# Optimization experiments

Measured on AMD Instinct MI355X. Metric: run time of the kernel, lower is better.

## Reference

```python
import jax, jax.numpy as jnp
import numpy as np

B, SQ, SK = 2, 2048, 2048   # batch, n_query, n_memory
D, H, DFF = 1024, 16, 1024  # model dim, heads, ffn dim (must equal D per source constraints)
DH = D // H                 # head dim = 64
NEG = 1e9


def _split_heads(x):
    # (B, S, D) -> (B, H, S, DH)
    b, s, _ = x.shape
    return x.reshape(b, s, H, DH).transpose(0, 2, 1, 3)


def setup_inputs() -> dict:
    key = jax.random.key(0)
    ks = jax.random.split(key, 10)
    s = 0.02
    return {
        "q": jax.random.normal(ks[0], (B, SQ, D), jnp.float32),
        "k": jax.random.normal(ks[1], (B, SK, D), jnp.float32),
        "v": jax.random.normal(ks[2], (B, SK, D), jnp.float32),
        "Win_w": jax.random.normal(ks[3], (DFF, D), jnp.float32) * s,
        "Win_b": jnp.zeros((DFF,), jnp.float32),
        "Wff_w": jax.random.normal(ks[4], (D, DFF), jnp.float32) * s,
        "Wff_b": jnp.zeros((D,), jnp.float32),
        "Wout_w": jax.random.normal(ks[5], (D, D), jnp.float32) * s,
        "Wout_b": jnp.zeros((D,), jnp.float32),
        "attn_mask": jax.random.randint(ks[6], (B, SK), 0, 2, jnp.int32),
    }


def reference(q, k, v, Win_w, Win_b, Wff_w, Wff_b, Wout_w, Wout_b, attn_mask):
    # projections (in_linear; k,v additionally pass through out_linear as in source)
    qh = q @ Win_w.T + Win_b
    kh = (k @ Win_w.T + Win_b) @ Wout_w.T + Wout_b
    vh = (v @ Win_w.T + Win_b) @ Wout_w.T + Wout_b
    qh = qh * (D ** -0.5)

    qh, kh, vh = _split_heads(qh), _split_heads(kh), _split_heads(vh)

    # additive mask bias: 0 where mask==1, -1e9 where mask==0, broadcast over heads/queries
    bias = (attn_mask.astype(jnp.float32) - 1.0) * NEG  # (B, SK)
    scores = jnp.einsum("bhqd,bhkd->bhqk", qh, kh) + bias[:, None, None, :]
    probs = jax.nn.softmax(scores, axis=-1)
    out = jnp.einsum("bhqk,bhkd->bhqd", probs, vh)

    # merge heads: (B, H, SQ, DH) -> (B, SQ, D)
    out = out.transpose(0, 2, 1, 3).reshape(B, SQ, D)

    out = out @ Wff_w.T + Wff_b
    out = out @ Wout_w.T + Wout_b
    return out
```

## Files before the change

kernel.cpp:

```cpp
#include <hip/hip_runtime.h>
#include <cstdint>
#include <cstddef>

using u16 = unsigned short;
using u32 = unsigned int;

typedef __attribute__((ext_vector_type(8))) short short8;
typedef __attribute__((ext_vector_type(4))) float f32x4;

#define MFMA16(a, b, c) __builtin_amdgcn_mfma_f32_16x16x32_bf16((a), (b), (c), 0, 0, 0)

#define QSCALE 0.0450842200f

__device__ __forceinline__ u16 f2bf(float f) {
  u32 u = __float_as_uint(f);
  return (u16)((u + 0x7FFFu + ((u >> 16) & 1u)) >> 16);
}

__device__ __forceinline__ u32 pack_bf16(float a, float b) {
  u32 r;
  asm("v_cvt_pk_bf16_f32 %0, %1, %2" : "=v"(r) : "v"(a), "v"(b));
  return r;
}

__device__ __forceinline__ void gload_lds16(const u16* g, u16* l) {
  __builtin_amdgcn_global_load_lds((const __attribute__((address_space(1))) void*)g,
                                   (__attribute__((address_space(3))) void*)l, 16, 0, 0);
}

__global__ __launch_bounds__(256) void prep_all(
    const float* __restrict__ q, const float* __restrict__ k, const float* __restrict__ v,
    const float* __restrict__ Wout_w, const float* __restrict__ Win_w,
    const float* __restrict__ Wff_w, const float* __restrict__ Win_b,
    const float* __restrict__ Wout_b, u16* __restrict__ X,
    u16* __restrict__ Woutb, u16* __restrict__ Winb,
    u16* __restrict__ WinT, u16* __restrict__ WffT,
    float* __restrict__ bias2, float* __restrict__ bias1f) {
  __shared__ float tile[64][68];
  const int t = threadIdx.x;
  const int bid = blockIdx.x;
  if (bid < 12288) {
    int i4 = bid * 256 + t;
    const float* src = (i4 < 1048576) ? q : (i4 < 2097152) ? k : v;
    int loc = i4 & 1048575;
    float4 w = reinterpret_cast<const float4*>(src)[loc];
    u32 lo = (u32)f2bf(w.x) | ((u32)f2bf(w.y) << 16);
    u32 hi = (u32)f2bf(w.z) | ((u32)f2bf(w.w) << 16);
    reinterpret_cast<uint2*>(X)[i4] = make_uint2(lo, hi);
  } else if (bid < 14336) {
    const int wb = bid - 12288;
    const float* src = wb < 1024 ? Wout_w : Win_w;
    u16* dst = wb < 1024 ? Woutb : Winb;
    const float sc = wb < 1024 ? 1.0f : QSCALE;
    int i = (wb & 1023) * 256 + t;
    float4 vv = reinterpret_cast<const float4*>(src)[i];
    u32 lo = (u32)f2bf(vv.x * sc) | ((u32)f2bf(vv.y * sc) << 16);
    u32 hi = (u32)f2bf(vv.z * sc) | ((u32)f2bf(vv.w * sc) << 16);
    reinterpret_cast<uint2*>(dst)[i] = make_uint2(lo, hi);
  } else if (bid < 14848) {
    const int tb = bid - 14336;
    const float* in = tb < 256 ? Win_w : Wff_w;
    u16* out = tb < 256 ? WinT : WffT;
    const int tix = tb & 255;
    const int bx = (tix >> 4) * 64, by = (tix & 15) * 64;
    const int r = t >> 2, c16 = (t & 3) * 16;
#pragma unroll
    for (int i = 0; i < 4; ++i)
      *reinterpret_cast<float4*>(&tile[r][c16 + i * 4]) =
          *reinterpret_cast<const float4*>(&in[(size_t)(bx + r) * 1024 + by + c16 + i * 4]);
    __syncthreads();
    const int jj = t >> 2, i16 = (t & 3) * 16;
#pragma unroll
    for (int i = 0; i < 4; ++i) {
      uint2 p;
      p.x = (u32)f2bf(tile[i16 + i * 4 + 0][jj]) | ((u32)f2bf(tile[i16 + i * 4 + 1][jj]) << 16);
      p.y = (u32)f2bf(tile[i16 + i * 4 + 2][jj]) | ((u32)f2bf(tile[i16 + i * 4 + 3][jj]) << 16);
      *reinterpret_cast<uint2*>(&out[(size_t)(by + jj) * 1024 + bx + i16 + i * 4]) = p;
    }
  } else if (bid < 15104) {
    const int w = t >> 6, l = t & 63;
    const int j = (bid - 14848) * 4 + w;
    const float4* Wr = reinterpret_cast<const float4*>(Wout_w + (size_t)j * 1024);
    const float4* br = reinterpret_cast<const float4*>(Win_b);
    float s = 0.f;
    for (int i = l; i < 256; i += 64) {
      float4 a = Wr[i], b = br[i];
      s += a.x * b.x + a.y * b.y + a.z * b.z + a.w * b.w;
    }
#pragma unroll
    for (int o = 1; o < 64; o <<= 1) s += __shfl_xor(s, o);
    if (l == 0) bias2[j] = s + Wout_b[j];
  } else {
    float4 vv = reinterpret_cast<const float4*>(Win_b)[t];
    vv.x *= QSCALE; vv.y *= QSCALE; vv.z *= QSCALE; vv.w *= QSCALE;
    reinterpret_cast<float4*>(bias1f)[t] = vv;
  }
}

__global__ __launch_bounds__(256) void gemm_w2(const u16* __restrict__ A,
                                               const u16* __restrict__ Bt0,
                                               const u16* __restrict__ Bt1,
                                               u16* __restrict__ C0,
                                               u16* __restrict__ C1) {
  const int bid = blockIdx.x;
  const int xcd = bid & 7, local = bid >> 3;
  const int z = local >> 5;
  const int mt = xcd * 2 + ((local >> 4) & 1);
  const int nt = local & 15;
  const u16* Bt = z ? Bt1 : Bt0;
  u16* C = z ? C1 : C0;
  __shared__ __align__(16) u16 As[2][4096];
  __shared__ __align__(16) u16 Bs[2][4096];
  const int t = threadIdx.x, w = t >> 6, l = t & 63;
  const int l15 = l & 15, l4 = l >> 4;
  const int m0 = mt * 64, n0 = nt * 64;
  f32x4 acc[4] = {};
  const int row0 = t >> 3, cs0 = t & 7;
  const int c0 = cs0 ^ (row0 & 7);
  const int row1 = row0 + 32;
  const int c1 = cs0 ^ (row1 & 7);
  const u16* gA0 = A + (size_t)(m0 + row0) * 1024 + c0 * 8;
  const u16* gA1 = A + (size_t)(m0 + row1) * 1024 + c1 * 8;
  const u16* gB0 = Bt + (size_t)(n0 + row0) * 1024 + c0 * 8;
  const u16* gB1 = Bt + (size_t)(n0 + row1) * 1024 + c1 * 8;
#define W2_STAGE(KK, DST)                             \
  gload_lds16(gA0 + (KK), &As[DST][0] + w * 512);     \
  gload_lds16(gA1 + (KK), &As[DST][2048] + w * 512);  \
  gload_lds16(gB0 + (KK), &Bs[DST][0] + w * 512);     \
  gload_lds16(gB1 + (KK), &Bs[DST][2048] + w * 512);
  W2_STAGE(0, 0)
  for (int step = 0; step < 16; ++step) {
    const int c = step & 1;
    __syncthreads();
    if (step < 15) { W2_STAGE((step + 1) * 64, c ^ 1) }
#pragma unroll
    for (int ks = 0; ks < 2; ++ks) {
      const int cc = ks * 4 + l4;
      short8 bfr = *reinterpret_cast<const short8*>(&Bs[c][(w * 16 + l15) * 64 + ((cc ^ (l15 & 7)) * 8)]);
#pragma unroll
      for (int i = 0; i < 4; ++i) {
        short8 afr = *reinterpret_cast<const short8*>(&As[c][(i * 16 + l15) * 64 + ((cc ^ (l15 & 7)) * 8)]);
        acc[i] = MFMA16(afr, bfr, acc[i]);
      }
    }
  }
#pragma unroll
  for (int i = 0; i < 4; ++i)
#pragma unroll
    for (int j = 0; j < 4; ++j)
      C[(size_t)(m0 + i * 16 + l4 * 4 + j) * 1024 + n0 + w * 16 + l15] = f2bf(acc[i][j]);
}

__global__ __launch_bounds__(256) void proj(const u16* __restrict__ X,
                                            const u16* __restrict__ Winb,
                                            const u16* __restrict__ Wc2,
                                            const float* __restrict__ bias1f,
                                            const float* __restrict__ bias2,
                                            u16* __restrict__ Qh,
                                            u16* __restrict__ Kp,
                                            u16* __restrict__ VT) {
  __shared__ __align__(16) u16 As[2][4096];
  __shared__ __align__(16) u16 Bs[2][4096];
  const int t = threadIdx.x, w = t >> 6, l = t & 63;
  const int l15 = l & 15, l4 = l >> 4;
  const int bid = blockIdx.x;
  const int xcd = bid & 7, local = bid >> 3;
  const int mt = xcd * 12 + (local >> 3);
  const int nt = local & 7;
  const int seg = mt >> 5;
  const int m0 = mt * 128;
  const int n0 = nt * 128;
  const int wr = (w >> 1) * 64, wc = (w & 1) * 64;
  const u16* Bt = seg == 0 ? Winb : Wc2;
  const float* bias = seg == 0 ? bias1f : bias2;

  f32x4 acc[4][4] = {};
  const u16* gA = X + (size_t)(m0 + (t >> 2)) * 1024 + (t & 3) * 8;
  const u16* gB = Bt + (size_t)(n0 + (t >> 2)) * 1024 + (t & 3) * 8;
#define PJ_STAGE(KK, DST)                                   \
  gload_lds16(gA + (KK), &As[DST][0] + w * 512);            \
  gload_lds16(gA + (KK) + 65536, &As[DST][2048] + w * 512); \
  gload_lds16(gB + (KK), &Bs[DST][0] + w * 512);            \
  gload_lds16(gB + (KK) + 65536, &Bs[DST][2048] + w * 512);
  PJ_STAGE(0, 0)
  for (int step = 0; step < 32; ++step) {
    const int c = step & 1;
    __syncthreads();
    if (step < 31) { PJ_STAGE((step + 1) * 32, c ^ 1) }
    short8 af[4], bf[4];
#pragma unroll
    for (int i = 0; i < 4; ++i)
      af[i] = *reinterpret_cast<const short8*>(&As[c][(wr + i * 16 + l15) * 32 + l4 * 8]);
#pragma unroll
    for (int i = 0; i < 4; ++i)
      bf[i] = *reinterpret_cast<const short8*>(&Bs[c][(wc + i * 16 + l15) * 32 + l4 * 8]);
#pragma unroll
    for (int mi = 0; mi < 4; ++mi)
#pragma unroll
      for (int ni = 0; ni < 4; ++ni)
        acc[mi][ni] = MFMA16(af[mi], bf[ni], acc[mi][ni]);
  }

#pragma unroll
  for (int mi = 0; mi < 4; ++mi) {
#pragma unroll
    for (int ni = 0; ni < 4; ++ni) {
      const int col = n0 + wc + ni * 16 + l15;
      const float bv = bias[col];
      const int row0 = m0 + wr + mi * 16 + l4 * 4;
      if (seg == 0) {
#pragma unroll
        for (int j = 0; j < 4; ++j)
          Qh[(size_t)(row0 + j) * 1024 + col] = f2bf(acc[mi][ni][j] + bv);
      } else if (seg == 1) {
#pragma unroll
        for (int j = 0; j < 4; ++j)
          Kp[(size_t)(row0 - 4096 + j) * 1024 + col] = f2bf(acc[mi][ni][j] + bv);
      } else {
        const int r = row0 - 8192;
        const int bb = r >> 11;
        const int sk = r & 2047;
        u32 p0 = (u32)f2bf(acc[mi][ni][0] + bv) | ((u32)f2bf(acc[mi][ni][1] + bv) << 16);
        u32 p1 = (u32)f2bf(acc[mi][ni][2] + bv) | ((u32)f2bf(acc[mi][ni][3] + bv) << 16);
        *reinterpret_cast<uint2*>(VT + ((size_t)(bb * 1024 + col)) * 2048 + sk) = make_uint2(p0, p1);
      }
    }
  }
}

__global__ __launch_bounds__(512) void attn(const u16* __restrict__ Qh,
                                            const u16* __restrict__ Kb,
                                            const u16* __restrict__ VT,
                                            const int* __restrict__ mask,
                                            u16* __restrict__ AO,
                                            const float* __restrict__ Wout_w,
                                            const float* __restrict__ Wff_b,
                                            const float* __restrict__ Wout_b,
                                            float* __restrict__ bias3) {
  __shared__ __align__(16) u16 Kt[128 * 64];
  __shared__ __align__(16) u16 Vt[2][64 * 64];
  __shared__ __align__(16) u16 Pw[8 * 16 * 64];
  __shared__ float biasS[2048];
  const int t = threadIdx.x, l = t & 63, w = t >> 6;
  const int bid = blockIdx.x;

  if (bid >= 512) {
    const int j = (bid - 512) * 8 + w;
    const float4* Wr = reinterpret_cast<const float4*>(Wout_w + (size_t)j * 1024);
    const float4* br = reinterpret_cast<const float4*>(Wff_b);
    float s = 0.f;
    for (int i = l; i < 256; i += 64) {
      float4 a = Wr[i], b = br[i];
      s += a.x * b.x + a.y * b.y + a.z * b.z + a.w * b.w;
    }
#pragma unroll
    for (int o = 1; o < 64; o <<= 1) s += __shfl_xor(s, o);
    if (l == 0) bias3[j] = s + Wout_b[j];
    return;
  }

  const int l15 = l & 15, l4 = l >> 4;
  const int bh = (bid & 7) * 4 + ((bid >> 3) & 3);
  const int qb = bid >> 5;
  const int b = bh >> 4, h = bh & 15, q0 = qb * 128;

  for (int i = t; i < 2048; i += 512) biasS[i] = mask[b * 2048 + i] ? 0.f : -1.442695e9f;

  short8 qf[2];
  {
    const u16* qp = Qh + (size_t)(b * 2048 + q0 + w * 16 + l15) * 1024 + h * 64 + l4 * 8;
    qf[0] = *reinterpret_cast<const short8*>(qp);
    qf[1] = *reinterpret_cast<const short8*>(qp + 32);
  }
  short8 ones;
#pragma unroll
  for (int i = 0; i < 8; ++i) ones[i] = (short)0x3F80;

  f32x4 acc[4] = {};
  f32x4 accS = {};

  const int rr = t >> 3, cs = t & 7;
  const int ck = cs ^ (rr & 7);
  const u16* gK = Kb + (size_t)(b * 2048 + rr) * 1024 + h * 64 + ck * 8;
  u16* ldsK = Kt + w * 512;
  const u32* gV = reinterpret_cast<const u32*>(VT) + (size_t)(b * 1024 + h * 64 + rr) * 1024 + ck;
  const int pws = w * 1024;

  for (int kt = 0; kt < 2048; kt += 128) {
    const u32* gvt = gV + (kt >> 1);
    u32 A0 = gvt[0], A1 = gvt[8], A2 = gvt[16], A3 = gvt[24];
    u32 B0 = gvt[32], B1 = gvt[40], B2 = gvt[48], B3 = gvt[56];
    __syncthreads();
    gload_lds16(gK + (size_t)kt * 1024, ldsK);
    gload_lds16(gK + (size_t)(kt + 64) * 1024, ldsK + 4096);
    uint4 vv;
    vv.x = (A0 & 0xffffu) | (A1 << 16);
    vv.y = (A2 & 0xffffu) | (A3 << 16);
    vv.z = (A0 >> 16) | (A1 & 0xffff0000u);
    vv.w = (A2 >> 16) | (A3 & 0xffff0000u);
    *reinterpret_cast<uint4*>(&Vt[0][rr * 64 + cs * 8]) = vv;
    vv.x = (B0 & 0xffffu) | (B1 << 16);
    vv.y = (B2 & 0xffffu) | (B3 << 16);
    vv.z = (B0 >> 16) | (B1 & 0xffff0000u);
    vv.w = (B2 >> 16) | (B3 & 0xffff0000u);
    *reinterpret_cast<uint4*>(&Vt[1][rr * 64 + cs * 8]) = vv;
    __syncthreads();

#pragma unroll
    for (int half = 0; half < 2; ++half) {
      const int kb0 = kt + half * 64;
      f32x4 s[4] = {};
      __builtin_amdgcn_s_setprio(1);
#pragma unroll
      for (int ks = 0; ks < 2; ++ks) {
        const int cc = ks * 4 + l4;
#pragma unroll
        for (int n = 0; n < 4; ++n) {
          short8 kb = *reinterpret_cast<const short8*>(
              &Kt[(half * 64 + n * 16 + l15) * 64 + ((cc ^ (l15 & 7)) * 8)]);
          s[n] = MFMA16(qf[ks], kb, s[n]);
        }
      }
      __builtin_amdgcn_s_setprio(0);
#pragma unroll
      for (int n = 0; n < 4; ++n) {
        const float bv = biasS[kb0 + n * 16 + l15];
#pragma unroll
        for (int j = 0; j < 4; ++j) s[n][j] = __builtin_amdgcn_exp2f(s[n][j] + bv);
      }
#pragma unroll
      for (int j = 0; j < 4; ++j) {
        const int r = l4 * 4 + j;
        uint2 pk;
        pk.x = pack_bf16(s[0][j], s[1][j]);
        pk.y = pack_bf16(s[2][j], s[3][j]);
        *reinterpret_cast<uint2*>(
            &Pw[pws + r * 64 + (((l15 >> 1) ^ (r & 7)) * 8) + (l15 & 1) * 4]) = pk;
      }
      __builtin_amdgcn_s_setprio(1);
#pragma unroll
      for (int ks = 0; ks < 2; ++ks) {
        const int cc = ks * 4 + l4;
        short8 pa = *reinterpret_cast<const short8*>(&Pw[pws + l15 * 64 + ((cc ^ (l15 & 7)) * 8)]);
#pragma unroll
        for (int n = 0; n < 4; ++n) {
          short8 vb = *reinterpret_cast<const short8*>(
              &Vt[half][(n * 16 + l15) * 64 + ((cc ^ (l15 & 7)) * 8)]);
          acc[n] = MFMA16(pa, vb, acc[n]);
        }
        accS = MFMA16(pa, ones, accS);
      }
      __builtin_amdgcn_s_setprio(0);
    }
  }

  const size_t orow0 = (size_t)(b * 2048 + q0 + w * 16 + l4 * 4);
#pragma unroll
  for (int j = 0; j < 4; ++j) {
    const float inv = 1.0f / accS[j];
#pragma unroll
    for (int n = 0; n < 4; ++n)
      AO[(orow0 + j) * 1024 + h * 64 + n * 16 + l15] = f2bf(acc[n][j] * inv);
  }
}

__global__ __launch_bounds__(256) void gemm_tail(const u16* __restrict__ A,
                                                 const u16* __restrict__ Bt,
                                                 const float* __restrict__ bias,
                                                 float* __restrict__ C) {
  __shared__ __align__(16) u16 As[2][4096];
  __shared__ __align__(16) u16 Bs[2][2048];
  const int t = threadIdx.x, w = t >> 6, l = t & 63;
  const int l15 = l & 15, l4 = l >> 4;
  const int bid = blockIdx.x;
  const int xcd = bid & 7, local = bid >> 3;
  const int mt = xcd * 4 + (local >> 4);
  const int nt = local & 15;
  const int m0 = mt * 128, n0 = nt * 64;
  const int wr = (w >> 1) * 64, wc = (w & 1) * 32;
  f32x4 acc[4][2] = {};
  const u16* gA = A + (size_t)(m0 + (t >> 2)) * 1024 + (t & 3) * 8;
  const u16* gB = Bt + (size_t)(n0 + (t >> 2)) * 1024 + (t & 3) * 8;
#define TL_STAGE(KK, DST)                                   \
  gload_lds16(gA + (KK), &As[DST][0] + w * 512);            \
  gload_lds16(gA + (KK) + 65536, &As[DST][2048] + w * 512); \
  gload_lds16(gB + (KK), &Bs[DST][0] + w * 512);
  TL_STAGE(0, 0)
  for (int step = 0; step < 32; ++step) {
    const int c = step & 1;
    __syncthreads();
    if (step < 31) { TL_STAGE((step + 1) * 32, c ^ 1) }
    short8 af[4], bf[2];
#pragma unroll
    for (int i = 0; i < 4; ++i)
      af[i] = *reinterpret_cast<const short8*>(&As[c][(wr + i * 16 + l15) * 32 + l4 * 8]);
#pragma unroll
    for (int i = 0; i < 2; ++i)
      bf[i] = *reinterpret_cast<const short8*>(&Bs[c][(wc + i * 16 + l15) * 32 + l4 * 8]);
#pragma unroll
    for (int mi = 0; mi < 4; ++mi)
#pragma unroll
      for (int ni = 0; ni < 2; ++ni)
        acc[mi][ni] = MFMA16(af[mi], bf[ni], acc[mi][ni]);
  }
#pragma unroll
  for (int mi = 0; mi < 4; ++mi) {
#pragma unroll
    for (int ni = 0; ni < 2; ++ni) {
      const int col = n0 + wc + ni * 16 + l15;
      const float bv = bias[col];
      const int row0 = m0 + wr + mi * 16 + l4 * 4;
#pragma unroll
      for (int j = 0; j < 4; ++j)
        C[(size_t)(row0 + j) * 1024 + col] = acc[mi][ni][j] + bv;
    }
  }
}

extern "C" void kernel_launch(void* const* d_in, const int* in_sizes, int n_in,
                              void* d_out, int out_size, void* d_ws, size_t ws_size,
                              hipStream_t stream) {
  const float* q = (const float*)d_in[0];
  const float* k = (const float*)d_in[1];
  const float* v = (const float*)d_in[2];
  const float* Win_w = (const float*)d_in[3];
  const float* Win_b = (const float*)d_in[4];
  const float* Wff_w = (const float*)d_in[5];
  const float* Wff_b = (const float*)d_in[6];
  const float* Wout_w = (const float*)d_in[7];
  const float* Wout_b = (const float*)d_in[8];
  const int* mask = (const int*)d_in[9];
  float* out = (float*)d_out;

  char* ws = (char*)d_ws;
  u16* Xbf = (u16*)ws;
  u16* AO = (u16*)ws;
  float* bias3 = (float*)(ws + 20971520);
  u16* Qh = (u16*)(ws + 25165824);
  u16* WinT = (u16*)(ws + 25165824);
  u16* Woutb = (u16*)(ws + 27262976);
  u16* WffT = (u16*)(ws + 29360128);
  u16* Kproj = (u16*)(ws + 33554432);
  u16* VT = (u16*)(ws + 41943040);
  u16* Wc2 = (u16*)(ws + 50331648);
  u16* Wc3 = (u16*)(ws + 52428800);
  u16* Winb = (u16*)(ws + 54525952);
  float* bias2 = out;
  float* bias1f = out + 1024;

  prep_all<<<15105, 256, 0, stream>>>(q, k, v, Wout_w, Win_w, Wff_w, Win_b, Wout_b,
                                      Xbf, Woutb, Winb, WinT, WffT, bias2, bias1f);
  gemm_w2<<<512, 256, 0, stream>>>(Woutb, WinT, WffT, Wc2, Wc3);
  proj<<<768, 256, 0, stream>>>(Xbf, Winb, Wc2, bias1f, bias2, Qh, Kproj, VT);
  attn<<<640, 512, 0, stream>>>(Qh, Kproj, VT, mask, AO, Wout_w, Wff_b, Wout_b, bias3);
  gemm_tail<<<512, 256, 0, stream>>>(AO, Wc3, bias3, out);
}
```

Measured before the change: 146.6 us.

## Keep attention probabilities in registers by transposing the score MFMA

Swaps the operands of the QK^T MFMA so each lane holds score values along the key dimension, which lets the exp'd probabilities be packed directly into the A-operand registers for the PV MFMA. This removes the per-warp LDS staging buffer for P and its write/read round trip. The mask bias is preloaded as the MFMA accumulator initial value, and the V tile load is changed to wider uint2 loads with a permuted key order that matches the new P register layout. It depends on the key permutation within V, P and K staying consistent, and a layout mismatch would give wrong results.

```diff
diff --git a/kernel.cpp b/kernel.cpp
--- a/kernel.cpp
+++ b/kernel.cpp
@@ -239,7 +239,6 @@
                                             float* __restrict__ bias3) {
   __shared__ __align__(16) u16 Kt[128 * 64];
   __shared__ __align__(16) u16 Vt[2][64 * 64];
-  __shared__ __align__(16) u16 Pw[8 * 16 * 64];
   __shared__ float biasS[2048];
   const int t = threadIdx.x, l = t & 63, w = t >> 6;
   const int bid = blockIdx.x;
@@ -281,35 +280,31 @@
 
   const int rr = t >> 3, cs = t & 7;
   const int ck = cs ^ (rr & 7);
+  const int vb = (ck >> 2) * 32 + (ck & 3) * 4;
   const u16* gK = Kb + (size_t)(b * 2048 + rr) * 1024 + h * 64 + ck * 8;
   u16* ldsK = Kt + w * 512;
-  const u32* gV = reinterpret_cast<const u32*>(VT) + (size_t)(b * 1024 + h * 64 + rr) * 1024 + ck;
-  const int pws = w * 1024;
+  const u32* gVrow = reinterpret_cast<const u32*>(VT) + (size_t)(b * 1024 + h * 64 + rr) * 1024;
 
   for (int kt = 0; kt < 2048; kt += 128) {
-    const u32* gvt = gV + (kt >> 1);
-    u32 A0 = gvt[0], A1 = gvt[8], A2 = gvt[16], A3 = gvt[24];
-    u32 B0 = gvt[32], B1 = gvt[40], B2 = gvt[48], B3 = gvt[56];
+    const int ia = (kt >> 1) + (vb >> 1);
+    uint2 a01 = *reinterpret_cast<const uint2*>(gVrow + ia);
+    uint2 a89 = *reinterpret_cast<const uint2*>(gVrow + ia + 8);
+    uint2 b01 = *reinterpret_cast<const uint2*>(gVrow + ia + 32);
+    uint2 b89 = *reinterpret_cast<const uint2*>(gVrow + ia + 40);
     __syncthreads();
     gload_lds16(gK + (size_t)kt * 1024, ldsK);
     gload_lds16(gK + (size_t)(kt + 64) * 1024, ldsK + 4096);
-    uint4 vv;
-    vv.x = (A0 & 0xffffu) | (A1 << 16);
-    vv.y = (A2 & 0xffffu) | (A3 << 16);
-    vv.z = (A0 >> 16) | (A1 & 0xffff0000u);
-    vv.w = (A2 >> 16) | (A3 & 0xffff0000u);
-    *reinterpret_cast<uint4*>(&Vt[0][rr * 64 + cs * 8]) = vv;
-    vv.x = (B0 & 0xffffu) | (B1 << 16);
-    vv.y = (B2 & 0xffffu) | (B3 << 16);
-    vv.z = (B0 >> 16) | (B1 & 0xffff0000u);
-    vv.w = (B2 >> 16) | (B3 & 0xffff0000u);
-    *reinterpret_cast<uint4*>(&Vt[1][rr * 64 + cs * 8]) = vv;
+    *reinterpret_cast<uint4*>(&Vt[0][rr * 64 + cs * 8]) = make_uint4(a01.x, a01.y, a89.x, a89.y);
+    *reinterpret_cast<uint4*>(&Vt[1][rr * 64 + cs * 8]) = make_uint4(b01.x, b01.y, b89.x, b89.y);
     __syncthreads();
 
 #pragma unroll
     for (int half = 0; half < 2; ++half) {
       const int kb0 = kt + half * 64;
-      f32x4 s[4] = {};
+      f32x4 s[4];
+#pragma unroll
+      for (int n = 0; n < 4; ++n)
+        s[n] = *reinterpret_cast<const f32x4*>(&biasS[kb0 + n * 16 + l4 * 4]);
       __builtin_amdgcn_s_setprio(1);
 #pragma unroll
       for (int ks = 0; ks < 2; ++ks) {
@@ -318,35 +313,35 @@
         for (int n = 0; n < 4; ++n) {
           short8 kb = *reinterpret_cast<const short8*>(
               &Kt[(half * 64 + n * 16 + l15) * 64 + ((cc ^ (l15 & 7)) * 8)]);
-          s[n] = MFMA16(qf[ks], kb, s[n]);
+          s[n] = MFMA16(kb, qf[ks], s[n]);
         }
       }
       __builtin_amdgcn_s_setprio(0);
 #pragma unroll
-      for (int n = 0; n < 4; ++n) {
-        const float bv = biasS[kb0 + n * 16 + l15];
-#pragma unroll
-        for (int j = 0; j < 4; ++j) s[n][j] = __builtin_amdgcn_exp2f(s[n][j] + bv);
-      }
-#pragma unroll
-      for (int j = 0; j < 4; ++j) {
-        const int r = l4 * 4 + j;
-        uint2 pk;
-        pk.x = pack_bf16(s[0][j], s[1][j]);
-        pk.y = pack_bf16(s[2][j], s[3][j]);
-        *reinterpret_cast<uint2*>(
-            &Pw[pws + r * 64 + (((l15 >> 1) ^ (r & 7)) * 8) + (l15 & 1) * 4]) = pk;
-      }
+      for (int n = 0; n < 4; ++n)
+#pragma unroll
+        for (int j = 0; j < 4; ++j) s[n][j] = __builtin_amdgcn_exp2f(s[n][j]);
+      u32 paw[8];
+      paw[0] = pack_bf16(s[0][0], s[0][1]);
+      paw[1] = pack_bf16(s[0][2], s[0][3]);
+      paw[2] = pack_bf16(s[1][0], s[1][1]);
+      paw[3] = pack_bf16(s[1][2], s[1][3]);
+      paw[4] = pack_bf16(s[2][0], s[2][1]);
+      paw[5] = pack_bf16(s[2][2], s[2][3]);
+      paw[6] = pack_bf16(s[3][0], s[3][1]);
+      paw[7] = pack_bf16(s[3][2], s[3][3]);
+      const short8 pa0 = *reinterpret_cast<const short8*>(&paw[0]);
+      const short8 pa1 = *reinterpret_cast<const short8*>(&paw[4]);
       __builtin_amdgcn_s_setprio(1);
 #pragma unroll
       for (int ks = 0; ks < 2; ++ks) {
+        const short8 pa = ks ? pa1 : pa0;
         const int cc = ks * 4 + l4;
-        short8 pa = *reinterpret_cast<const short8*>(&Pw[pws + l15 * 64 + ((cc ^ (l15 & 7)) * 8)]);
 #pragma unroll
         for (int n = 0; n < 4; ++n) {
-          short8 vb = *reinterpret_cast<const short8*>(
+          short8 vb8 = *reinterpret_cast<const short8*>(
               &Vt[half][(n * 16 + l15) * 64 + ((cc ^ (l15 & 7)) * 8)]);
-          acc[n] = MFMA16(pa, vb, acc[n]);
+          acc[n] = MFMA16(pa, vb8, acc[n]);
         }
         accS = MFMA16(pa, ones, accS);
       }
```

Measured after the change: 141.9 us. 1.03x faster.
